# Kernel optimization log

Measured on AMD Instinct MI355X. Metric: run time of the kernel, lower is better.

## Reference

```python
import jax, jax.numpy as jnp
import numpy as np

CAUSAL = True
SOFTMAX_SCALE = 0.125
K_DIFF = 192
MASK_FILL = -1000000.0


def setup_inputs() -> dict:
    key = jax.random.key(0)
    ks = jax.random.split(key, 5)
    shape = (1, 8, 192, 64)  # [batch, n_heads, seq, head_dim]
    return {
        "q": jax.random.normal(ks[0], shape, dtype=jnp.float32),
        "k1": jax.random.normal(ks[1], shape, dtype=jnp.float32),
        "k2": jax.random.normal(ks[2], shape, dtype=jnp.float32),
        "v1": jax.random.normal(ks[3], shape, dtype=jnp.float32),
        "v2": jax.random.normal(ks[4], shape, dtype=jnp.float32),
    }


def reference(q, k1, k2, v1, v2):
    b, n, S, h = q.shape
    # Third-order (trittention) scores.
    score_qk = jnp.einsum("bnth,bnqh->bntq", k2, q)   # [b,n,t,q]
    score_kk = jnp.einsum("bnsh,bnth->bnst", k1, k2)  # [b,n,s,t]
    # score[b,n,s,t,q] = score_kk[b,n,s,t] + score_qk[b,n,t,q]
    score = score_kk[..., None] + score_qk[:, :, None, :, :]
    if CAUSAL:
        # Torch mask (dims named t,s,q over score dims s,t,q):
        # masked where s_score > t_score, t_score > q_score, or t_score - s_score > k_diff
        s_i = jnp.arange(S)[:, None, None]
        t_i = jnp.arange(S)[None, :, None]
        q_i = jnp.arange(S)[None, None, :]
        mask = (s_i > t_i) | (t_i > q_i) | (t_i - s_i > K_DIFF)
        score = jnp.where(mask, MASK_FILL, score)
    pre_softmax_attn_score = score  # [b,n,s,t,q]
    # Rearrange 'b n s t q -> b n q (s t)' and scale.
    flat = jnp.transpose(score, (0, 1, 4, 2, 3)).reshape(b, n, S, S * S) * SOFTMAX_SCALE
    M0 = jnp.max(flat, axis=-1)                       # [b,n,q]
    p = jax.nn.softmax(flat, axis=-1)                  # standard softmax (no +0.01)
    L = jnp.sum(jnp.exp(flat - M0[..., None]), axis=-1) + 0.01
    M = M0 + jnp.log(L)                                # non-standard LSE with +0.01
    # SiLU-gated value combination: v[b,n,s,t,h] = silu(v1[s]) * v2[t]
    v_gated = jax.nn.silu(v1)[:, :, :, None, :] * v2[:, :, None, :, :]
    v_flat = jnp.transpose(v_gated, (0, 1, 4, 2, 3)).reshape(b, n, h, S * S)
    z = jnp.einsum("bnql,bnhl->bnqh", p, v_flat)
    return (z, pre_softmax_attn_score, v_gated, M)
```

## Files before the change

### kernel.cpp

```cpp
#include <hip/hip_runtime.h>
#include <math.h>

#define S 192
#define H 64
#define NH 8
#define SC 0.125f
#define FILLV (-1000000.0f)

typedef float floatx4 __attribute__((ext_vector_type(4)));

__device__ __forceinline__ float wave_max(float v) {
#pragma unroll
  for (int m = 32; m; m >>= 1) v = fmaxf(v, __shfl_xor(v, m));
  return v;
}
__device__ __forceinline__ float wave_sum(float v) {
#pragma unroll
  for (int m = 32; m; m >>= 1) v += __shfl_xor(v, m);
  return v;
}

__global__ void prep_kernel(const float* __restrict__ q, const float* __restrict__ k1,
                            const float* __restrict__ k2, const float* __restrict__ v1,
                            float* __restrict__ kk, float* __restrict__ qk,
                            float* __restrict__ sv1) {
  int b = blockIdx.x;
  if (b < 576) {
    bool is_kk = (b < 288);
    int bb = is_kk ? b : b - 288;
    int n = bb / 36;
    int rem = bb % 36;
    int rt = (rem / 6) * 32;
    int ct = (rem % 6) * 32;
    const float* Abase = (is_kk ? k1 : k2) + n * S * H;
    const float* Bbase = (is_kk ? k2 : q) + n * S * H;
    float* out = (is_kk ? kk : qk) + n * S * S;

    __shared__ float As[32][65];
    __shared__ float Bs[32][65];
    int tid = threadIdx.x;
    for (int i = tid; i < 32 * 64; i += 256) {
      int r = i >> 6, h = i & 63;
      As[r][h] = Abase[(rt + r) * H + h];
      Bs[r][h] = Bbase[(ct + r) * H + h];
    }
    __syncthreads();
    int r0 = (tid / 16) * 2, c0 = (tid % 16) * 2;
    float a00 = 0.f, a01 = 0.f, a10 = 0.f, a11 = 0.f;
#pragma unroll
    for (int h = 0; h < 64; ++h) {
      float x0 = As[r0][h], x1 = As[r0 + 1][h];
      float y0 = Bs[c0][h], y1 = Bs[c0 + 1][h];
      a00 += x0 * y0; a01 += x0 * y1; a10 += x1 * y0; a11 += x1 * y1;
    }
    out[(rt + r0) * S + ct + c0]         = a00;
    out[(rt + r0) * S + ct + c0 + 1]     = a01;
    out[(rt + r0 + 1) * S + ct + c0]     = a10;
    out[(rt + r0 + 1) * S + ct + c0 + 1] = a11;
  } else {
    int i = (b - 576) * 256 + threadIdx.x;
    const float4* v4 = (const float4*)v1;
    float4 x = v4[i];
    float4 y;
    y.x = x.x / (1.f + expf(-x.x));
    y.y = x.y / (1.f + expf(-x.y));
    y.z = x.z / (1.f + expf(-x.z));
    y.w = x.w / (1.f + expf(-x.w));
    ((float4*)sv1)[i] = y;
  }
}

__global__ __launch_bounds__(256) void stats_kernel(
    const float* __restrict__ kk, const float* __restrict__ sv1,
    float* __restrict__ mt, float* __restrict__ St, float* __restrict__ Aw) {
  int n = blockIdx.x / S, t = blockIdx.x % S;
  int tid = threadIdx.x, wv = tid >> 6, lane = tid & 63;
  __shared__ float w[S];
  __shared__ float red[4];
  __shared__ float part[4][H];
  const float* kkc = kk + n * S * S + t;

  float lm = -3.4e38f;
  for (int s = tid; s <= t; s += 256) lm = fmaxf(lm, SC * kkc[s * S]);
  lm = wave_max(lm);
  if (lane == 0) red[wv] = lm;
  __syncthreads();
  float m = fmaxf(fmaxf(red[0], red[1]), fmaxf(red[2], red[3]));

  float ls = 0.f;
  for (int s = tid; s <= t; s += 256) {
    float e = expf(SC * kkc[s * S] - m);
    w[s] = e;
    ls += e;
  }
  ls = wave_sum(ls);
  __syncthreads();
  if (lane == 0) red[wv] = ls;
  __syncthreads();
  float Ssum = red[0] + red[1] + red[2] + red[3];
  if (tid == 0) { mt[n * S + t] = m; St[n * S + t] = Ssum; }

  const float* sh = sv1 + n * S * H + lane;
  float acc = 0.f;
  for (int s = wv; s <= t; s += 4) acc += w[s] * sh[s * H];
  part[wv][lane] = acc;
  __syncthreads();
  if (wv == 0)
    Aw[(n * S + t) * H + lane] = part[0][lane] + part[1][lane] + part[2][lane] + part[3][lane];
}

__global__ __launch_bounds__(256) void out_kernel(
    const float* __restrict__ qk, const float* __restrict__ v2,
    const float* __restrict__ mt, const float* __restrict__ St,
    const float* __restrict__ Aw,
    float* __restrict__ z, float* __restrict__ Mout) {
  int n = blockIdx.x / S, qq = blockIdx.x % S;
  int tid = threadIdx.x, wv = tid >> 6, lane = tid & 63;
  __shared__ float e[S];
  __shared__ float red[4];
  __shared__ float part[4][H];
  const float* qkc = qk + n * S * S + qq;
  const float* mtp = mt + n * S;
  const float* Stp = St + n * S;

  float lm = -3.4e38f;
  for (int t = tid; t <= qq; t += 256) lm = fmaxf(lm, SC * qkc[t * S] + mtp[t]);
  lm = wave_max(lm);
  if (lane == 0) red[wv] = lm;
  __syncthreads();
  float M0 = fmaxf(fmaxf(red[0], red[1]), fmaxf(red[2], red[3]));

  float ls = 0.f;
  for (int t = tid; t <= qq; t += 256) {
    float ev = expf(SC * qkc[t * S] + mtp[t] - M0);
    e[t] = ev;
    ls += ev * Stp[t];
  }
  ls = wave_sum(ls);
  __syncthreads();
  if (lane == 0) red[wv] = ls;
  __syncthreads();
  float D = red[0] + red[1] + red[2] + red[3];
  if (tid == 0) Mout[n * S + qq] = M0 + logf(D + 0.01f);

  const float* vh = v2 + n * S * H + lane;
  const float* Ah = Aw + n * S * H + lane;
  float acc = 0.f;
  for (int t = wv; t <= qq; t += 4) acc += e[t] * vh[t * H] * Ah[t * H];
  part[wv][lane] = acc;
  __syncthreads();
  if (wv == 0)
    z[(n * S + qq) * H + lane] =
        (part[0][lane] + part[1][lane] + part[2][lane] + part[3][lane]) / D;
}

__global__ __launch_bounds__(512) void score_kernel(
    const float* __restrict__ kk, const float* __restrict__ qk,
    float* __restrict__ score) {
  int n = blockIdx.x / S, s = blockIdx.x % S;
  const float* kkr = kk + (n * S + s) * S;
  const float4* qk4 = (const float4*)(qk + n * S * S);
  floatx4* out4 = (floatx4*)(score + (size_t)(n * S + s) * S * S);

  for (int i = threadIdx.x; i < S * 48; i += 512) {
    int t = i / 48, j = i - t * 48;
    floatx4 v;
    if (t < s) {
      v = (floatx4){FILLV, FILLV, FILLV, FILLV};
    } else {
      float kv = kkr[t];
      float4 qv = qk4[t * 48 + j];
      int q0 = 4 * j;
      v.x = (t > q0)     ? FILLV : kv + qv.x;
      v.y = (t > q0 + 1) ? FILLV : kv + qv.y;
      v.z = (t > q0 + 2) ? FILLV : kv + qv.z;
      v.w = (t > q0 + 3) ? FILLV : kv + qv.w;
    }
    __builtin_nontemporal_store(v, &out4[i]);
  }
}

__global__ __launch_bounds__(256) void vg_kernel(
    const float* __restrict__ sv1, const float* __restrict__ v2,
    float* __restrict__ vg) {
  int n = blockIdx.x / S, s = blockIdx.x % S;
  const float4* a4 = (const float4*)(sv1 + (n * S + s) * H);
  const float4* b4 = (const float4*)(v2 + n * S * H);
  floatx4* out4 = (floatx4*)(vg + (size_t)(n * S + s) * S * H);

  for (int i = threadIdx.x; i < S * 16; i += 256) {
    int t = i >> 4, j = i & 15;
    float4 a = a4[j];
    float4 b = b4[t * 16 + j];
    floatx4 v = (floatx4){a.x * b.x, a.y * b.y, a.z * b.z, a.w * b.w};
    __builtin_nontemporal_store(v, &out4[i]);
  }
}

extern "C" void kernel_launch(void* const* d_in, const int* in_sizes, int n_in,
                              void* d_out, int out_size, void* d_ws, size_t ws_size,
                              hipStream_t stream) {
  const float* q  = (const float*)d_in[0];
  const float* k1 = (const float*)d_in[1];
  const float* k2 = (const float*)d_in[2];
  const float* v1 = (const float*)d_in[3];
  const float* v2 = (const float*)d_in[4];
  float* out = (float*)d_out;

  float* z     = out;
  float* score = out + 98304;
  float* vg    = out + 98304 + 56623104;
  float* Mout  = out + 98304 + 56623104 + 18874368;

  float* ws  = (float*)d_ws;
  float* kk  = ws;
  float* qk  = ws + 294912;
  float* sv1 = ws + 589824;
  float* mt  = ws + 688128;
  float* St  = ws + 689664;
  float* Aw  = ws + 691200;

  prep_kernel<<<dim3(672), dim3(256), 0, stream>>>(q, k1, k2, v1, kk, qk, sv1);
  stats_kernel<<<dim3(NH * S), dim3(256), 0, stream>>>(kk, sv1, mt, St, Aw);
  out_kernel<<<dim3(NH * S), dim3(256), 0, stream>>>(qk, v2, mt, St, Aw, z, Mout);
  score_kernel<<<dim3(NH * S), dim3(512), 0, stream>>>(kk, qk, score);
  vg_kernel<<<dim3(NH * S), dim3(256), 0, stream>>>(sv1, v2, vg);
}
```

Baseline: 356.9 us.

## Add transposed score matrices and fuse score/vgated writers into one kernel

The prep kernel now also computes transposed copies of kk and qk, so the stats and output kernels read contiguous rows instead of strided columns. The score and v_gated writer kernels are merged into a single launch with 384-thread blocks, and the loops are restructured with fixed trip counts and unrolling. Nontemporal stores are replaced by plain stores. This removes one launch and the uncoalesced reads, at the cost of extra GEMM work and workspace; dropping the nontemporal hints may change cache behaviour on the large output write.

```diff
diff --git a/kernel.cpp b/kernel.cpp
--- a/kernel.cpp
+++ b/kernel.cpp
@@ -7,8 +7,6 @@
 #define SC 0.125f
 #define FILLV (-1000000.0f)
 
-typedef float floatx4 __attribute__((ext_vector_type(4)));
-
 __device__ __forceinline__ float wave_max(float v) {
 #pragma unroll
   for (int m = 32; m; m >>= 1) v = fmaxf(v, __shfl_xor(v, m));
@@ -20,21 +18,26 @@
   return v;
 }
 
-__global__ void prep_kernel(const float* __restrict__ q, const float* __restrict__ k1,
-                            const float* __restrict__ k2, const float* __restrict__ v1,
-                            float* __restrict__ kk, float* __restrict__ qk,
-                            float* __restrict__ sv1) {
+__global__ __launch_bounds__(256) void prep_kernel(
+    const float* __restrict__ q, const float* __restrict__ k1,
+    const float* __restrict__ k2, const float* __restrict__ v1,
+    float* __restrict__ kk, float* __restrict__ qk,
+    float* __restrict__ kkT, float* __restrict__ qkT,
+    float* __restrict__ sv1) {
   int b = blockIdx.x;
-  if (b < 576) {
-    bool is_kk = (b < 288);
-    int bb = is_kk ? b : b - 288;
-    int n = bb / 36;
-    int rem = bb % 36;
+  if (b < 1152) {
+    int p = b / 288, bb = b % 288;
+    int n = bb / 36, rem = bb % 36;
     int rt = (rem / 6) * 32;
     int ct = (rem % 6) * 32;
-    const float* Abase = (is_kk ? k1 : k2) + n * S * H;
-    const float* Bbase = (is_kk ? k2 : q) + n * S * H;
-    float* out = (is_kk ? kk : qk) + n * S * S;
+    const float* Abase;
+    const float* Bbase;
+    float* out;
+    if (p == 0)      { Abase = k1; Bbase = k2; out = kk; }
+    else if (p == 1) { Abase = k2; Bbase = q;  out = qk; }
+    else if (p == 2) { Abase = k2; Bbase = k1; out = kkT; }
+    else             { Abase = q;  Bbase = k2; out = qkT; }
+    Abase += n * S * H; Bbase += n * S * H; out += n * S * S;
 
     __shared__ float As[32][65];
     __shared__ float Bs[32][65];
@@ -58,7 +61,7 @@
     out[(rt + r0 + 1) * S + ct + c0]     = a10;
     out[(rt + r0 + 1) * S + ct + c0 + 1] = a11;
   } else {
-    int i = (b - 576) * 256 + threadIdx.x;
+    int i = (b - 1152) * 256 + threadIdx.x;
     const float4* v4 = (const float4*)v1;
     float4 x = v4[i];
     float4 y;
@@ -71,17 +74,17 @@
 }
 
 __global__ __launch_bounds__(256) void stats_kernel(
-    const float* __restrict__ kk, const float* __restrict__ sv1,
+    const float* __restrict__ kkT, const float* __restrict__ sv1,
     float* __restrict__ mt, float* __restrict__ St, float* __restrict__ Aw) {
   int n = blockIdx.x / S, t = blockIdx.x % S;
   int tid = threadIdx.x, wv = tid >> 6, lane = tid & 63;
   __shared__ float w[S];
   __shared__ float red[4];
   __shared__ float part[4][H];
-  const float* kkc = kk + n * S * S + t;
+  const float* kkr = kkT + n * S * S + t * S;
 
   float lm = -3.4e38f;
-  for (int s = tid; s <= t; s += 256) lm = fmaxf(lm, SC * kkc[s * S]);
+  for (int s = tid; s <= t; s += 256) lm = fmaxf(lm, SC * kkr[s]);
   lm = wave_max(lm);
   if (lane == 0) red[wv] = lm;
   __syncthreads();
@@ -89,7 +92,7 @@
 
   float ls = 0.f;
   for (int s = tid; s <= t; s += 256) {
-    float e = expf(SC * kkc[s * S] - m);
+    float e = expf(SC * kkr[s] - m);
     w[s] = e;
     ls += e;
   }
@@ -110,7 +113,7 @@
 }
 
 __global__ __launch_bounds__(256) void out_kernel(
-    const float* __restrict__ qk, const float* __restrict__ v2,
+    const float* __restrict__ qkT, const float* __restrict__ v2,
     const float* __restrict__ mt, const float* __restrict__ St,
     const float* __restrict__ Aw,
     float* __restrict__ z, float* __restrict__ Mout) {
@@ -119,12 +122,12 @@
   __shared__ float e[S];
   __shared__ float red[4];
   __shared__ float part[4][H];
-  const float* qkc = qk + n * S * S + qq;
+  const float* qkr = qkT + n * S * S + qq * S;
   const float* mtp = mt + n * S;
   const float* Stp = St + n * S;
 
   float lm = -3.4e38f;
-  for (int t = tid; t <= qq; t += 256) lm = fmaxf(lm, SC * qkc[t * S] + mtp[t]);
+  for (int t = tid; t <= qq; t += 256) lm = fmaxf(lm, SC * qkr[t] + mtp[t]);
   lm = wave_max(lm);
   if (lane == 0) red[wv] = lm;
   __syncthreads();
@@ -132,7 +135,7 @@
 
   float ls = 0.f;
   for (int t = tid; t <= qq; t += 256) {
-    float ev = expf(SC * qkc[t * S] + mtp[t] - M0);
+    float ev = expf(SC * qkr[t] + mtp[t] - M0);
     e[t] = ev;
     ls += ev * Stp[t];
   }
@@ -154,46 +157,47 @@
         (part[0][lane] + part[1][lane] + part[2][lane] + part[3][lane]) / D;
 }
 
-__global__ __launch_bounds__(512) void score_kernel(
+__global__ __launch_bounds__(384) void stream_kernel(
     const float* __restrict__ kk, const float* __restrict__ qk,
-    float* __restrict__ score) {
-  int n = blockIdx.x / S, s = blockIdx.x % S;
-  const float* kkr = kk + (n * S + s) * S;
-  const float4* qk4 = (const float4*)(qk + n * S * S);
-  floatx4* out4 = (floatx4*)(score + (size_t)(n * S + s) * S * S);
-
-  for (int i = threadIdx.x; i < S * 48; i += 512) {
-    int t = i / 48, j = i - t * 48;
-    floatx4 v;
-    if (t < s) {
-      v = (floatx4){FILLV, FILLV, FILLV, FILLV};
-    } else {
+    const float* __restrict__ sv1, const float* __restrict__ v2,
+    float* __restrict__ score, float* __restrict__ vg) {
+  int b = blockIdx.x;
+  int tid = threadIdx.x;
+  if (b < 1536) {
+    int n = b / S, s = b % S;
+    const float* kkr = kk + (n * S + s) * S;
+    const float4* qk4 = (const float4*)(qk + n * S * S);
+    float4* out4 = (float4*)(score + (size_t)(n * S + s) * S * S);
+    int r = tid / 48;
+    int j = tid % 48;
+    int q0 = 4 * j;
+#pragma unroll 4
+    for (int tbase = 0; tbase < S; tbase += 8) {
+      int t = tbase + r;
       float kv = kkr[t];
       float4 qv = qk4[t * 48 + j];
-      int q0 = 4 * j;
-      v.x = (t > q0)     ? FILLV : kv + qv.x;
-      v.y = (t > q0 + 1) ? FILLV : kv + qv.y;
-      v.z = (t > q0 + 2) ? FILLV : kv + qv.z;
-      v.w = (t > q0 + 3) ? FILLV : kv + qv.w;
-    }
-    __builtin_nontemporal_store(v, &out4[i]);
-  }
-}
-
-__global__ __launch_bounds__(256) void vg_kernel(
-    const float* __restrict__ sv1, const float* __restrict__ v2,
-    float* __restrict__ vg) {
-  int n = blockIdx.x / S, s = blockIdx.x % S;
-  const float4* a4 = (const float4*)(sv1 + (n * S + s) * H);
-  const float4* b4 = (const float4*)(v2 + n * S * H);
-  floatx4* out4 = (floatx4*)(vg + (size_t)(n * S + s) * S * H);
-
-  for (int i = threadIdx.x; i < S * 16; i += 256) {
-    int t = i >> 4, j = i & 15;
-    float4 a = a4[j];
-    float4 b = b4[t * 16 + j];
-    floatx4 v = (floatx4){a.x * b.x, a.y * b.y, a.z * b.z, a.w * b.w};
-    __builtin_nontemporal_store(v, &out4[i]);
+      bool rowmask = (t < s);
+      float4 v;
+      v.x = (rowmask || t > q0)     ? FILLV : kv + qv.x;
+      v.y = (rowmask || t > q0 + 1) ? FILLV : kv + qv.y;
+      v.z = (rowmask || t > q0 + 2) ? FILLV : kv + qv.z;
+      v.w = (rowmask || t > q0 + 3) ? FILLV : kv + qv.w;
+      out4[t * 48 + j] = v;
+    }
+  } else {
+    int bb = b - 1536;
+    int n = bb / S, s = bb % S;
+    const float4* a4 = (const float4*)(sv1 + (n * S + s) * H);
+    const float4* b4 = (const float4*)(v2 + n * S * H);
+    float4* out4 = (float4*)(vg + (size_t)(n * S + s) * S * H);
+#pragma unroll
+    for (int it = 0; it < 8; ++it) {
+      int i = it * 384 + tid;
+      int t = i >> 4, j = i & 15;
+      float4 a = a4[j];
+      float4 bv = b4[t * 16 + j];
+      out4[i] = make_float4(a.x * bv.x, a.y * bv.y, a.z * bv.z, a.w * bv.w);
+    }
   }
 }
 
@@ -212,17 +216,18 @@
   float* vg    = out + 98304 + 56623104;
   float* Mout  = out + 98304 + 56623104 + 18874368;
 
-  float* ws  = (float*)d_ws;
-  float* kk  = ws;
-  float* qk  = ws + 294912;
-  float* sv1 = ws + 589824;
-  float* mt  = ws + 688128;
-  float* St  = ws + 689664;
-  float* Aw  = ws + 691200;
-
-  prep_kernel<<<dim3(672), dim3(256), 0, stream>>>(q, k1, k2, v1, kk, qk, sv1);
-  stats_kernel<<<dim3(NH * S), dim3(256), 0, stream>>>(kk, sv1, mt, St, Aw);
-  out_kernel<<<dim3(NH * S), dim3(256), 0, stream>>>(qk, v2, mt, St, Aw, z, Mout);
-  score_kernel<<<dim3(NH * S), dim3(512), 0, stream>>>(kk, qk, score);
-  vg_kernel<<<dim3(NH * S), dim3(256), 0, stream>>>(sv1, v2, vg);
-}
+  float* ws   = (float*)d_ws;
+  float* kk   = ws;
+  float* qk   = ws + 294912;
+  float* kkT  = ws + 589824;
+  float* qkT  = ws + 884736;
+  float* sv1  = ws + 1179648;
+  float* mt   = ws + 1277952;
+  float* St   = ws + 1279488;
+  float* Aw   = ws + 1281024;
+
+  prep_kernel<<<dim3(1248), dim3(256), 0, stream>>>(q, k1, k2, v1, kk, qk, kkT, qkT, sv1);
+  stats_kernel<<<dim3(NH * S), dim3(256), 0, stream>>>(kkT, sv1, mt, St, Aw);
+  out_kernel<<<dim3(NH * S), dim3(256), 0, stream>>>(qkT, v2, mt, St, Aw, z, Mout);
+  stream_kernel<<<dim3(3072), dim3(384), 0, stream>>>(kk, qk, sv1, v2, score, vg);
+}
```

Result: no change. 358.7 us (+0.5%).
